# Kernel tuning notes

Hardware: AMD Instinct MI355X
Metric: run time of the kernel (lower is better)

## Reference

```python
import jax, jax.numpy as jnp
import numpy as np

B, S, T, E, H = 2, 2048, 2048, 1024, 16
D = E // H  # head_dim = 64


def setup_inputs() -> dict:
    key = jax.random.key(0)
    ks = jax.random.split(key, 11)
    scale = 1.0 / np.sqrt(E)
    return {
        "query": jax.random.normal(ks[0], (B, S, E), jnp.float32),
        "value": jax.random.normal(ks[1], (B, T, E), jnp.float32),
        "key": jax.random.normal(ks[2], (B, T, E), jnp.float32),
        "Wq": jax.random.normal(ks[3], (E, E), jnp.float32) * scale,
        "bq": jnp.zeros((E,), jnp.float32),
        "Wk": jax.random.normal(ks[4], (E, E), jnp.float32) * scale,
        "bk": jnp.zeros((E,), jnp.float32),
        "Wv": jax.random.normal(ks[5], (E, E), jnp.float32) * scale,
        "bv": jnp.zeros((E,), jnp.float32),
        "Wo": jax.random.normal(ks[6], (E, E), jnp.float32) * scale,
        "bo": jnp.zeros((E,), jnp.float32),
    }


def reference(query, value, key, Wq, bq, Wk, bk, Wv, bv, Wo, bo):
    b, s, e = query.shape
    t = value.shape[1]
    # linear projections (torch Linear: x @ W.T + b)
    q = query @ Wq.T + bq
    k = key @ Wk.T + bk
    v = value @ Wv.T + bv
    # split heads: [B, H, S, D]
    q = q.reshape(b, s, H, D).transpose(0, 2, 1, 3)
    k = k.reshape(b, t, H, D).transpose(0, 2, 1, 3)
    v = v.reshape(b, t, H, D).transpose(0, 2, 1, 3)
    # scaled dot-product attention; full [B,H,S,T] scores as in the original
    A = jnp.einsum("bhsd,bhtd->bhst", q, k) / jnp.sqrt(jnp.float32(D))
    A = jax.nn.softmax(A, axis=-1)
    # dropout p=0.0 -> identity
    out = jnp.einsum("bhst,bhtd->bhsd", A, v)
    out = out.transpose(0, 2, 1, 3).reshape(b, s, e)
    return out @ Wo.T + bo
```

## Files before the change

kernel.cpp:

```cpp
#include <hip/hip_runtime.h>
#include <math.h>

typedef __attribute__((ext_vector_type(8))) short short8;
typedef __attribute__((ext_vector_type(4))) float f32x4;
typedef __attribute__((ext_vector_type(16))) float f32x16;
typedef unsigned short u16;

__device__ __forceinline__ u16 f2bf(float x) {
    unsigned int u = __float_as_uint(x);
    u += 0x7FFFu + ((u >> 16) & 1u);
    return (u16)(u >> 16);
}

__device__ __forceinline__ unsigned cvt_pk_bf16(float lo, float hi) {
    unsigned r;
    asm("v_cvt_pk_bf16_f32 %0, %1, %2" : "=v"(r) : "v"(lo), "v"(hi));
    return r;
}

__device__ __forceinline__ void load_lds16(const void* g, void* l) {
    __builtin_amdgcn_global_load_lds(
        (const __attribute__((address_space(1))) unsigned int*)g,
        (__attribute__((address_space(3))) unsigned int*)l,
        16, 0, 0);
}

struct CvtArgs {
    const float* src[7];
    u16* dst[7];
    int n8[7];
};

__global__ __launch_bounds__(256) void cvt_bf16(CvtArgs c) {
    const int z = blockIdx.z;
    const int i = blockIdx.x * 256 + threadIdx.x;
    if (i >= c.n8[z]) return;
    const float4* s = (const float4*)c.src[z];
    const float4 a = s[2 * i];
    const float4 b = s[2 * i + 1];
    union { short8 v; unsigned u[4]; } o;
    o.u[0] = cvt_pk_bf16(a.x, a.y);
    o.u[1] = cvt_pk_bf16(a.z, a.w);
    o.u[2] = cvt_pk_bf16(b.x, b.y);
    o.u[3] = cvt_pk_bf16(b.z, b.w);
    ((short8*)c.dst[z])[i] = o.v;
}

struct GemmArgs {
    const u16* A[3];
    const u16* W[3];
    const float* bias[3];
    void* C[3];
    float scale[3];
    int trans[3];
};

template <bool BF16OUT>
__global__ __launch_bounds__(256) void gemm_nt_mfma(GemmArgs ga, int M, int N, int K)
{
    __shared__ u16 As[128 * 32];
    __shared__ u16 Bs[128 * 32];
    const int z = blockIdx.z;
    const u16* __restrict__ A = ga.A[z];
    const u16* __restrict__ W = ga.W[z];
    const float* __restrict__ bias = ga.bias[z];
    const float scale = ga.scale[z];
    const int trans = ga.trans[z];

    const int tid = threadIdx.x;
    const int w = tid >> 6, l = tid & 63;
    const int l4 = l >> 4, lm = l & 15;
    const int wr = w >> 1, wc = w & 1;

    const int idx = blockIdx.x;
    const int xcd = idx & 7;
    const int sl  = idx >> 3;
    const int bmi = xcd * 4 + (sl & 3);
    const int bni = sl >> 2;
    const int bm = (trans ? bni : bmi) * 128;
    const int bn = (trans ? bmi : bni) * 128;

    const int srow = l >> 2;
    const int sseg = l & 3;

    f32x4 acc[4][4];
#pragma unroll
    for (int m = 0; m < 4; ++m)
#pragma unroll
        for (int n = 0; n < 4; ++n) acc[m][n] = (f32x4){0.f, 0.f, 0.f, 0.f};

    for (int k0 = 0; k0 < K; k0 += 32) {
        __syncthreads();
#pragma unroll
        for (int i = 0; i < 2; ++i) {
            const int blk = w * 2 + i;
            const int row = blk * 16 + srow;
            load_lds16(A + (size_t)(bm + row) * K + k0 + sseg * 8,
                       (char*)As + blk * 1024);
            load_lds16(W + (size_t)(bn + row) * K + k0 + sseg * 8,
                       (char*)Bs + blk * 1024);
        }
        __syncthreads();

        short8 af[4], bf[4];
#pragma unroll
        for (int m = 0; m < 4; ++m)
            af[m] = *(const short8*)&As[(wr * 64 + m * 16 + lm) * 32 + l4 * 8];
#pragma unroll
        for (int n = 0; n < 4; ++n)
            bf[n] = *(const short8*)&Bs[(wc * 64 + n * 16 + lm) * 32 + l4 * 8];
#pragma unroll
        for (int m = 0; m < 4; ++m)
#pragma unroll
            for (int n = 0; n < 4; ++n)
                acc[m][n] = __builtin_amdgcn_mfma_f32_16x16x32_bf16(af[m], bf[n], acc[m][n], 0, 0, 0);
    }

    if (!trans) {
        float bv[4];
#pragma unroll
        for (int n = 0; n < 4; ++n) bv[n] = bias[bn + wc * 64 + n * 16 + lm];
#pragma unroll
        for (int m = 0; m < 4; ++m) {
#pragma unroll
            for (int n = 0; n < 4; ++n) {
                const int col = bn + wc * 64 + n * 16 + lm;
#pragma unroll
                for (int r = 0; r < 4; ++r) {
                    const int row = bm + wr * 64 + m * 16 + l4 * 4 + r;
                    const float v = (acc[m][n][r] + bv[n]) * scale;
                    if (BF16OUT)
                        ((u16*)ga.C[z])[(size_t)row * N + col] = f2bf(v);
                    else
                        ((float*)ga.C[z])[(size_t)row * N + col] = v;
                }
            }
        }
    } else {
#pragma unroll
        for (int m = 0; m < 4; ++m) {
            const float4 bv4 = *(const float4*)(bias + bm + wr * 64 + m * 16 + l4 * 4);
            const float bvr[4] = {bv4.x, bv4.y, bv4.z, bv4.w};
#pragma unroll
            for (int n = 0; n < 4; ++n) {
                const int col = bn + wc * 64 + n * 16 + lm;
                const size_t cbase = (size_t)(col >> 11) * 2097152 + (size_t)(col & 2047);
#pragma unroll
                for (int r = 0; r < 4; ++r) {
                    const int row = bm + wr * 64 + m * 16 + l4 * 4 + r;
                    const float v = (acc[m][n][r] + bvr[r]) * scale;
                    ((u16*)ga.C[z])[cbase + (size_t)row * 2048] = f2bf(v);
                }
            }
        }
    }
}

__global__ __launch_bounds__(256, 2) void flash_attn_mfma9(
    const u16* __restrict__ Qb, const u16* __restrict__ Kb,
    const u16* __restrict__ Vt, u16* __restrict__ Ob)
{
    __shared__ u16 Ks[2][128 * 64];
    __shared__ u16 Vs[2][64 * 128];

    const int tid = threadIdx.x;
    const int w  = tid >> 6;
    const int l  = tid & 63;
    const int hi = l >> 5;
    const int lq = l & 31;

    const int id = blockIdx.x;
    const int xcd = id & 7;
    const int s = id >> 3;
    const int qt = s & 15;
    const int g0 = (s >> 4) * 8 + xcd;
    const int h = g0 & 15;
    const int b = g0 >> 4;
    const int qb0 = qt << 7;

    const size_t bbase = (size_t)b * 2048 * 1024 + (size_t)h * 64;
    const size_t vbase = (size_t)b * 2097152 + (size_t)(h * 64) * 2048;

    short8 qf[4];
    {
        const u16* qrow = Qb + bbase + (size_t)(qb0 + w * 32 + lq) * 1024;
#pragma unroll
        for (int t = 0; t < 4; ++t)
            qf[t] = *(const short8*)(qrow + t * 16 + hi * 8);
    }

    auto stageK = [&](int t0, int bufi) {
#pragma unroll
        for (int ii = 0; ii < 4; ++ii) {
            const int i = w * 4 + ii;
            const int key = i * 8 + (l >> 3);
            const int chunk = (l & 7) ^ ((l >> 3) & 7);
            load_lds16(Kb + bbase + (size_t)(t0 + key) * 1024 + chunk * 8,
                       (char*)&Ks[bufi][0] + i * 1024);
        }
    };
    auto stageV = [&](int t0, int bufi) {
#pragma unroll
        for (int ii = 0; ii < 4; ++ii) {
            const int i = w * 4 + ii;
            const int d = i * 4 + (l >> 4);
            const int chunk = (l & 15) ^ (d & 7);
            load_lds16(Vt + vbase + (size_t)d * 2048 + t0 + chunk * 8,
                       (char*)&Vs[bufi][0] + i * 1024);
        }
    };

    f32x16 oacc[2] = {{}, {}};
    float m_run = -1e30f;
    float l_run = 0.f;

    stageK(0, 0);
    stageV(0, 0);

    for (int t = 0; t < 16; ++t) {
        const int buf = t & 1;
        if (t < 15) {
            stageK((t + 1) * 128, buf ^ 1);
            stageV((t + 1) * 128, buf ^ 1);
            asm volatile("s_waitcnt vmcnt(8)" ::: "memory");
        } else {
            asm volatile("s_waitcnt vmcnt(0)" ::: "memory");
        }
        __builtin_amdgcn_s_barrier();

        f32x16 sacc[4] = {{}, {}, {}, {}};
        __builtin_amdgcn_s_setprio(1);
#pragma unroll
        for (int kb = 0; kb < 4; ++kb) {
#pragma unroll
            for (int tt = 0; tt < 4; ++tt) {
                const short8 kf = *(const short8*)
                    &Ks[buf][(32 * kb + lq) * 64 + (((2 * tt + hi) ^ (l & 7)) << 3)];
                sacc[kb] = __builtin_amdgcn_mfma_f32_32x32x16_bf16(kf, qf[tt], sacc[kb], 0, 0, 0);
            }
        }
        __builtin_amdgcn_s_setprio(0);

        float mt = sacc[0][0];
#pragma unroll
        for (int kb = 0; kb < 4; ++kb)
#pragma unroll
            for (int r = 0; r < 16; ++r)
                mt = fmaxf(mt, sacc[kb][r]);
        mt = fmaxf(mt, __shfl_xor(mt, 32));

        const bool resc = !__all(mt <= m_run + 8.0f);
        if (resc) {
            const float mn = fmaxf(m_run, mt);
            const float alpha = __builtin_amdgcn_exp2f(m_run - mn);
            m_run = mn;
            l_run *= alpha;
#pragma unroll
            for (int r = 0; r < 16; ++r) {
                const float a = __shfl(alpha, (r & 3) + 8 * (r >> 2) + 4 * hi);
                oacc[0][r] *= a;
                oacc[1][r] *= a;
            }
        }

        float lsum = 0.f;
        const float mr = m_run;
        unsigned wlo[4][4], whi[4][4];
#pragma unroll
        for (int kb = 0; kb < 4; ++kb) {
#pragma unroll
            for (int qd = 0; qd < 4; ++qd) {
                const float p0 = __builtin_amdgcn_exp2f(sacc[kb][4 * qd + 0] - mr);
                const float p1 = __builtin_amdgcn_exp2f(sacc[kb][4 * qd + 1] - mr);
                const float p2 = __builtin_amdgcn_exp2f(sacc[kb][4 * qd + 2] - mr);
                const float p3 = __builtin_amdgcn_exp2f(sacc[kb][4 * qd + 3] - mr);
                lsum += (p0 + p1) + (p2 + p3);
                wlo[kb][qd] = cvt_pk_bf16(p0, p1);
                whi[kb][qd] = cvt_pk_bf16(p2, p3);
            }
        }
        lsum += __shfl_xor(lsum, 32);
        l_run += lsum;

#pragma unroll
        for (int kb = 0; kb < 4; ++kb) {
#pragma unroll
            for (int u = 0; u < 2; ++u) {
                unsigned X  = wlo[kb][2 * u], Y  = wlo[kb][2 * u + 1];
                unsigned X2 = whi[kb][2 * u], Y2 = whi[kb][2 * u + 1];
                asm("v_permlane32_swap_b32 %0, %1" : "+v"(X),  "+v"(Y));
                asm("v_permlane32_swap_b32 %0, %1" : "+v"(X2), "+v"(Y2));
                union { unsigned u4[4]; short8 v8; } pa;
                pa.u4[0] = X; pa.u4[1] = X2; pa.u4[2] = Y; pa.u4[3] = Y2;
                const int sstep = 2 * kb + u;
                __builtin_amdgcn_s_setprio(1);
#pragma unroll
                for (int g = 0; g < 2; ++g) {
                    const int d = 32 * g + lq;
                    const short8 vf = *(const short8*)
                        &Vs[buf][d * 128 + (((2 * sstep + hi) ^ (d & 7)) << 3)];
                    oacc[g] = __builtin_amdgcn_mfma_f32_32x32x16_bf16(pa.v8, vf, oacc[g], 0, 0, 0);
                }
                __builtin_amdgcn_s_setprio(0);
            }
        }

        __builtin_amdgcn_s_barrier();
    }

#pragma unroll
    for (int r = 0; r < 16; ++r) {
        const int row = (r & 3) + 8 * (r >> 2) + 4 * hi;
        const float linv = 1.f / __shfl(l_run, row);
        const size_t orow = bbase + (size_t)(qb0 + w * 32 + row) * 1024;
        Ob[orow + lq]      = f2bf(oacc[0][r] * linv);
        Ob[orow + 32 + lq] = f2bf(oacc[1][r] * linv);
    }
}

extern "C" void kernel_launch(void* const* d_in, const int* in_sizes, int n_in,
                              void* d_out, int out_size, void* d_ws, size_t ws_size,
                              hipStream_t stream)
{
    const float* query = (const float*)d_in[0];
    const float* value = (const float*)d_in[1];
    const float* key   = (const float*)d_in[2];
    const float* Wq = (const float*)d_in[3];
    const float* bq = (const float*)d_in[4];
    const float* Wk = (const float*)d_in[5];
    const float* bk = (const float*)d_in[6];
    const float* Wv = (const float*)d_in[7];
    const float* bv = (const float*)d_in[8];
    const float* Wo = (const float*)d_in[9];
    const float* bo = (const float*)d_in[10];
    float* out = (float*)d_out;

    const int M = 2 * 2048;
    const int E = 1024;
    const size_t act = (size_t)M * E;
    const size_t wel = (size_t)E * E;

    u16* qc  = (u16*)d_ws;
    u16* kc  = qc + act;
    u16* vc  = kc + act;
    u16* wqb = vc + act;
    u16* wkb = wqb + wel;
    u16* wvb = wkb + wel;
    u16* wob = wvb + wel;
    u16* Qb  = wob + wel;
    u16* Kb  = Qb + act;
    u16* Vtb = Kb + act;
    u16* Ab  = Vtb + act;

    CvtArgs ca;
    ca.src[0] = query; ca.dst[0] = qc;  ca.n8[0] = (int)(act / 8);
    ca.src[1] = key;   ca.dst[1] = kc;  ca.n8[1] = (int)(act / 8);
    ca.src[2] = value; ca.dst[2] = vc;  ca.n8[2] = (int)(act / 8);
    ca.src[3] = Wq;    ca.dst[3] = wqb; ca.n8[3] = (int)(wel / 8);
    ca.src[4] = Wk;    ca.dst[4] = wkb; ca.n8[4] = (int)(wel / 8);
    ca.src[5] = Wv;    ca.dst[5] = wvb; ca.n8[5] = (int)(wel / 8);
    ca.src[6] = Wo;    ca.dst[6] = wob; ca.n8[6] = (int)(wel / 8);
    dim3 cgrid((unsigned)((act / 8 + 255) / 256), 1, 7);
    hipLaunchKernelGGL(cvt_bf16, cgrid, dim3(256), 0, stream, ca);

    const float SCALE_Q = 0.125f * 1.4426950408889634f;

    GemmArgs gq;
    gq.A[0] = qc;  gq.W[0] = wqb; gq.bias[0] = bq; gq.C[0] = Qb;  gq.scale[0] = SCALE_Q; gq.trans[0] = 0;
    gq.A[1] = kc;  gq.W[1] = wkb; gq.bias[1] = bk; gq.C[1] = Kb;  gq.scale[1] = 1.0f;    gq.trans[1] = 0;
    gq.A[2] = wvb; gq.W[2] = vc;  gq.bias[2] = bv; gq.C[2] = Vtb; gq.scale[2] = 1.0f;    gq.trans[2] = 1;
    hipLaunchKernelGGL((gemm_nt_mfma<true>), dim3(256, 1, 3), dim3(256), 0, stream, gq, M, E, E);

    hipLaunchKernelGGL(flash_attn_mfma9, dim3(512), dim3(256), 0, stream, Qb, Kb, Vtb, Ab);

    GemmArgs go;
    go.A[0] = Ab; go.W[0] = wob; go.bias[0] = bo; go.C[0] = out; go.scale[0] = 1.0f; go.trans[0] = 0;
    go.A[1] = Ab; go.W[1] = wob; go.bias[1] = bo; go.C[1] = out; go.scale[1] = 1.0f; go.trans[1] = 0;
    go.A[2] = Ab; go.W[2] = wob; go.bias[2] = bo; go.C[2] = out; go.scale[2] = 1.0f; go.trans[2] = 0;
    hipLaunchKernelGGL((gemm_nt_mfma<false>), dim3(256, 1, 1), dim3(256), 0, stream, go, M, E, E);
}
```

Measured before the change: 145.4 us.

## Double-buffer projection GEMM LDS tiles and use max3 tree for row max

```diff
diff --git a/kernel.cpp b/kernel.cpp
--- a/kernel.cpp
+++ b/kernel.cpp
@@ -15,6 +15,12 @@
 __device__ __forceinline__ unsigned cvt_pk_bf16(float lo, float hi) {
     unsigned r;
     asm("v_cvt_pk_bf16_f32 %0, %1, %2" : "=v"(r) : "v"(lo), "v"(hi));
+    return r;
+}
+
+__device__ __forceinline__ float max3f(float a, float b, float c) {
+    float r;
+    asm("v_max3_f32 %0, %1, %2, %3" : "=v"(r) : "v"(a), "v"(b), "v"(c));
     return r;
 }
 
@@ -58,8 +64,8 @@
 template <bool BF16OUT>
 __global__ __launch_bounds__(256) void gemm_nt_mfma(GemmArgs ga, int M, int N, int K)
 {
-    __shared__ u16 As[128 * 32];
-    __shared__ u16 Bs[128 * 32];
+    __shared__ u16 As[2][128 * 32];
+    __shared__ u16 Bs[2][128 * 32];
     const int z = blockIdx.z;
     const u16* __restrict__ A = ga.A[z];
     const u16* __restrict__ W = ga.W[z];
@@ -89,31 +95,45 @@
 #pragma unroll
         for (int n = 0; n < 4; ++n) acc[m][n] = (f32x4){0.f, 0.f, 0.f, 0.f};
 
-    for (int k0 = 0; k0 < K; k0 += 32) {
-        __syncthreads();
+    auto stage = [&](int k0, int bi) {
 #pragma unroll
         for (int i = 0; i < 2; ++i) {
             const int blk = w * 2 + i;
             const int row = blk * 16 + srow;
             load_lds16(A + (size_t)(bm + row) * K + k0 + sseg * 8,
-                       (char*)As + blk * 1024);
+                       (char*)&As[bi][0] + blk * 1024);
             load_lds16(W + (size_t)(bn + row) * K + k0 + sseg * 8,
-                       (char*)Bs + blk * 1024);
-        }
-        __syncthreads();
+                       (char*)&Bs[bi][0] + blk * 1024);
+        }
+    };
+
+    const int nIt = K / 32;
+    stage(0, 0);
+
+    for (int it = 0; it < nIt; ++it) {
+        const int buf = it & 1;
+        if (it < nIt - 1) {
+            stage((it + 1) * 32, buf ^ 1);
+            asm volatile("s_waitcnt vmcnt(4)" ::: "memory");
+        } else {
+            asm volatile("s_waitcnt vmcnt(0)" ::: "memory");
+        }
+        __builtin_amdgcn_s_barrier();
 
         short8 af[4], bf[4];
 #pragma unroll
         for (int m = 0; m < 4; ++m)
-            af[m] = *(const short8*)&As[(wr * 64 + m * 16 + lm) * 32 + l4 * 8];
+            af[m] = *(const short8*)&As[buf][(wr * 64 + m * 16 + lm) * 32 + l4 * 8];
 #pragma unroll
         for (int n = 0; n < 4; ++n)
-            bf[n] = *(const short8*)&Bs[(wc * 64 + n * 16 + lm) * 32 + l4 * 8];
+            bf[n] = *(const short8*)&Bs[buf][(wc * 64 + n * 16 + lm) * 32 + l4 * 8];
 #pragma unroll
         for (int m = 0; m < 4; ++m)
 #pragma unroll
             for (int n = 0; n < 4; ++n)
                 acc[m][n] = __builtin_amdgcn_mfma_f32_16x16x32_bf16(af[m], bf[n], acc[m][n], 0, 0, 0);
+
+        __builtin_amdgcn_s_barrier();
     }
 
     if (!trans) {
@@ -241,12 +261,20 @@
         }
         __builtin_amdgcn_s_setprio(0);
 
-        float mt = sacc[0][0];
-#pragma unroll
-        for (int kb = 0; kb < 4; ++kb)
-#pragma unroll
-            for (int r = 0; r < 16; ++r)
-                mt = fmaxf(mt, sacc[kb][r]);
+        float amax[4];
+#pragma unroll
+        for (int kb = 0; kb < 4; ++kb) {
+            const f32x16 sv = sacc[kb];
+            float t0 = max3f(sv[0], sv[1], sv[2]);
+            float t1 = max3f(sv[3], sv[4], sv[5]);
+            float t2 = max3f(sv[6], sv[7], sv[8]);
+            float t3 = max3f(sv[9], sv[10], sv[11]);
+            float t4 = max3f(sv[12], sv[13], sv[14]);
+            float u0 = max3f(t0, t1, t2);
+            float u1 = max3f(t3, t4, sv[15]);
+            amax[kb] = fmaxf(u0, u1);
+        }
+        float mt = fmaxf(max3f(amax[0], amax[1], amax[2]), amax[3]);
         mt = fmaxf(mt, __shfl_xor(mt, 32));
 
         const bool resc = !__all(mt <= m_run + 8.0f);
```

Result: faster. 137.6 us (median of 2 runs) (-5.4%).
